# Kernel tuning notes

Hardware: AMD Instinct MI355X
Metric: run time of the kernel (lower is better)

## Reference

```python
import jax, jax.numpy as jnp
import numpy as np

EPS = 1e-5          # InstanceNorm eps (torch default)
KERNEL = 25         # moving_avg_kernel_size
TAU = 1.0           # gumbel softmax temperature
REGIME_NUM = 8


def _inorm(x):
    # InstanceNorm1d without affine on (N, C, L): normalize over last dim (biased var)
    m = x.mean(-1, keepdims=True)
    v = ((x - m) ** 2).mean(-1, keepdims=True)
    return (x - m) * jax.lax.rsqrt(v + EPS)


def _lbr(x, W, b):
    # Linear -> InstanceNorm (over last dim) -> exact GELU
    return jax.nn.gelu(_inorm(x @ W + b), approximate=False)


def _moving_avg(x, k):
    # x: (B, L, C); edge-replicate pad (k-1)//2 on both sides, sliding mean via cumsum
    p = (k - 1) // 2
    xp = jnp.concatenate([jnp.repeat(x[:, :1], p, axis=1), x,
                          jnp.repeat(x[:, -1:], p, axis=1)], axis=1)
    cs = jnp.concatenate([jnp.zeros_like(xp[:, :1]), jnp.cumsum(xp, axis=1)], axis=1)
    return (cs[:, k:] - cs[:, :-k]) / k  # (B, L, C)


def _encode(x, Ws, bs, Wt, bt):
    # inputs - inputs[:, 0:1]; series decomposition; seasonal+trend branches
    x = x - x[:, :1]
    mm = _moving_avg(x, KERNEL)
    return _lbr(x - mm, Ws, bs) + _lbr(mm, Wt, bt)  # (B, L, H)


def reference(inputs_longterm, inputs_shortterm,
              Ws, bs, Wt, bt,
              Wh1, bh1, Wl1, bl1, Wh2, bh2, Wl2, bl2, Wh3, bh3, Wl3, bl3,
              Wr, br, proto):
    e_lt = _encode(inputs_longterm, Ws, bs, Wt, bt)   # (B, L_lt, H)
    e_st = _encode(inputs_shortterm, Ws, bs, Wt, bt)  # (B, L_st, H)

    # RegimeEncoder: alternate hidden-dim and lookback-dim LinearBatchRelu layers
    o = _lbr(e_lt, Wh1, bh1)
    o = jnp.swapaxes(_lbr(jnp.swapaxes(o, 1, 2), Wl1, bl1), 1, 2)
    o = _lbr(o, Wh2, bh2)
    o = jnp.swapaxes(_lbr(jnp.swapaxes(o, 1, 2), Wl2, bl2), 1, 2)
    o = _lbr(o, Wh3, bh3)
    o = jnp.swapaxes(_lbr(jnp.swapaxes(o, 1, 2), Wl3, bl3), 1, 2)  # (B, L_lt//8, H)
    logits = o.reshape(o.shape[0], -1) @ Wr + br  # (B, R)

    # gumbel_softmax(hard=True) with straight-through estimator
    g = jax.random.gumbel(jax.random.key(42), logits.shape, logits.dtype)
    y_soft = jax.nn.softmax((logits + g) / TAU, axis=-1)
    y_hard = jax.nn.one_hot(jnp.argmax(y_soft, axis=-1), REGIME_NUM, dtype=logits.dtype)
    w = y_hard - jax.lax.stop_gradient(y_soft) + y_soft  # (B, R)

    # weighted sum over regime prototypes, then combine with encoded shortterm
    sel = jnp.einsum('br,rnhmo->bnhmo', w, proto)          # (B, L_st, H, M, 3)
    out = jnp.einsum('bnh,bnhmo->bmo', e_st, sel)          # (B, M, 3)
    B = out.shape[0]
    return jax.nn.softmax(out.reshape(B, -1), axis=-1).reshape(out.shape)


def setup_inputs() -> dict:
    key = jax.random.key(0)
    ks = jax.random.split(key, 24)
    B, L_lt, L_st, C, H, R, M = 32, 512, 128, 9, 128, 8, 64
    s = 0.02
    d = {
        'inputs_longterm':  jax.random.normal(ks[0], (B, L_lt, C), jnp.float32),
        'inputs_shortterm': jax.random.normal(ks[1], (B, L_st, C), jnp.float32),
        'Ws': jax.random.normal(ks[2], (C, H), jnp.float32) * s,
        'bs': jnp.zeros((H,), jnp.float32),
        'Wt': jax.random.normal(ks[3], (C, H), jnp.float32) * s,
        'bt': jnp.zeros((H,), jnp.float32),
        'Wh1': jax.random.normal(ks[4], (H, H), jnp.float32) * s,
        'bh1': jnp.zeros((H,), jnp.float32),
        'Wl1': jax.random.normal(ks[5], (L_lt, L_lt // 2), jnp.float32) * s,
        'bl1': jnp.zeros((L_lt // 2,), jnp.float32),
        'Wh2': jax.random.normal(ks[6], (H, H), jnp.float32) * s,
        'bh2': jnp.zeros((H,), jnp.float32),
        'Wl2': jax.random.normal(ks[7], (L_lt // 2, L_lt // 4), jnp.float32) * s,
        'bl2': jnp.zeros((L_lt // 4,), jnp.float32),
        'Wh3': jax.random.normal(ks[8], (H, H), jnp.float32) * s,
        'bh3': jnp.zeros((H,), jnp.float32),
        'Wl3': jax.random.normal(ks[9], (L_lt // 4, L_lt // 8), jnp.float32) * s,
        'bl3': jnp.zeros((L_lt // 8,), jnp.float32),
        'Wr': jax.random.normal(ks[10], (H * L_lt // 8, R), jnp.float32) * s,
        'br': jnp.zeros((R,), jnp.float32),
        'proto': jax.random.normal(ks[11], (R, L_st, H, M, 3), jnp.float32),
    }
    return d
```

## Files before the change

### kernel.cpp

```cpp
#include <hip/hip_runtime.h>
#include <math.h>

#define EPS 1e-5f

__device__ __forceinline__ float gelu_exact(float x) {
    return 0.5f * x * (1.0f + erff(x * 0.7071067811865476f));
}

__device__ float block_sum(float v, float* red) {
    int lane = threadIdx.x & 63, wid = threadIdx.x >> 6;
#pragma unroll
    for (int off = 32; off > 0; off >>= 1) v += __shfl_down(v, off, 64);
    if (lane == 0) red[wid] = v;
    __syncthreads();
    int nw = ((int)blockDim.x + 63) >> 6;
    float s = red[0];
    for (int w = 1; w < nw; w++) s += red[w];
    __syncthreads();
    return s;
}

__device__ float block_max(float v, float* red) {
    int lane = threadIdx.x & 63, wid = threadIdx.x >> 6;
#pragma unroll
    for (int off = 32; off > 0; off >>= 1) v = fmaxf(v, __shfl_down(v, off, 64));
    if (lane == 0) red[wid] = v;
    __syncthreads();
    int nw = ((int)blockDim.x + 63) >> 6;
    float s = red[0];
    for (int w = 1; w < nw; w++) s = fmaxf(s, red[w]);
    __syncthreads();
    return s;
}

__device__ void threefry2x32(unsigned k0, unsigned k1, unsigned x0, unsigned x1,
                             unsigned& o0, unsigned& o1) {
    unsigned ks[3] = {k0, k1, k0 ^ k1 ^ 0x1BD11BDAu};
    const unsigned rot[2][4] = {{13u, 15u, 26u, 6u}, {17u, 29u, 16u, 24u}};
    x0 += ks[0]; x1 += ks[1];
#pragma unroll
    for (int i = 0; i < 5; i++) {
#pragma unroll
        for (int j = 0; j < 4; j++) {
            unsigned r = rot[i & 1][j];
            x0 += x1;
            x1 = (x1 << r) | (x1 >> (32 - r));
            x1 ^= x0;
        }
        x0 += ks[(i + 1) % 3];
        x1 += ks[(i + 2) % 3] + (unsigned)(i + 1);
    }
    o0 = x0; o1 = x1;
}

__device__ float gumbel_at(int j) {
    unsigned o0, o1;
    threefry2x32(0u, 42u, 0u, (unsigned)j, o0, o1);
    unsigned bits = o0 ^ o1;
    float f = __uint_as_float((bits >> 9) | 0x3F800000u) - 1.0f;
    float u = fmaxf(f + 1.17549435e-38f, 1.17549435e-38f);
    return -logf(-logf(u));
}

__device__ void bsum2_128(float& a, float& b, float (*red)[2]) {
    int lane = threadIdx.x & 63, wid = threadIdx.x >> 6;
#pragma unroll
    for (int off = 32; off > 0; off >>= 1) {
        a += __shfl_xor(a, off, 64);
        b += __shfl_xor(b, off, 64);
    }
    if (lane == 0) { red[wid][0] = a; red[wid][1] = b; }
    __syncthreads();
    a = red[0][0] + red[1][0];
    b = red[0][1] + red[1][1];
}

__global__ void encode_kernel(const float* __restrict__ x_lt, const float* __restrict__ x_st,
                              const float* __restrict__ Ws, const float* __restrict__ bs,
                              const float* __restrict__ Wt, const float* __restrict__ bt,
                              float* __restrict__ e_lt, float* __restrict__ e_st) {
    const int H = 128;
    int b = blockIdx.y, t = threadIdx.x;
    const float* x;
    float* e;
    int L, l;
    if (blockIdx.x < 512) { x = x_lt; e = e_lt; L = 512; l = blockIdx.x; }
    else { x = x_st; e = e_st; L = 128; l = blockIdx.x - 512; }
    __shared__ float part[117];
    __shared__ float seas[9], mmv[9];
    __shared__ float redA[2][2], redB[2][2];
    const float* xb = x + (size_t)b * L * 9;
    if (t < 117) {
        int c = t / 13, g = t % 13;
        int lj0 = l + 2 * g - 12;
        lj0 = lj0 < 0 ? 0 : (lj0 >= L ? L - 1 : lj0);
        float s = xb[(size_t)lj0 * 9 + c];
        if (g < 12) {
            int lj1 = l + 2 * g - 11;
            lj1 = lj1 < 0 ? 0 : (lj1 >= L ? L - 1 : lj1);
            s += xb[(size_t)lj1 * 9 + c];
        }
        part[t] = s;
    }
    __syncthreads();
    if (t < 9) {
        float s = 0.f;
        for (int g = 0; g < 13; g++) s += part[t * 13 + g];
        float x0 = xb[t];
        float mm = (s - 25.f * x0) * (1.0f / 25.0f);
        float xd = xb[(size_t)l * 9 + t] - x0;
        mmv[t] = mm;
        seas[t] = xd - mm;
    }
    __syncthreads();
    float ys = bs[t], yt = bt[t];
#pragma unroll
    for (int c = 0; c < 9; c++) {
        ys += seas[c] * Ws[c * H + t];
        yt += mmv[c] * Wt[c * H + t];
    }
    float sa = ys, sb = yt;
    bsum2_128(sa, sb, redA);
    float ms = sa * (1.0f / 128.0f), mt = sb * (1.0f / 128.0f);
    float ds = ys - ms, dt = yt - mt;
    float qa = ds * ds, qb = dt * dt;
    bsum2_128(qa, qb, redB);
    float gy = gelu_exact(ds * rsqrtf(qa * (1.0f / 128.0f) + EPS));
    float gt = gelu_exact(dt * rsqrtf(qb * (1.0f / 128.0f) + EPS));
    e[((size_t)b * L + l) * H + t] = gy + gt;
}

template <int K, int N, int WR, bool TRANS>
__global__ __launch_bounds__(256) void lbr_wave(
    const float* __restrict__ A, int S, int ABOFF,
    const float* __restrict__ W, const float* __restrict__ bias,
    float* __restrict__ out, int OROWS, int OBOFF) {
    constexpr int CG = N / 4;
    constexpr int SG = 64 / CG;
    constexpr int RW = SG * WR;
    constexpr int MT = 4 * RW;
    constexpr int LOG2MT = (MT == 8) ? 3 : ((MT == 16) ? 4 : 5);
    constexpr int STAGE = 4 * RW * K;
    constexpr int TILE = TRANS ? MT * (N + 4) : 0;
    constexpr int LSZ = STAGE > TILE ? STAGE : TILE;
    __shared__ float lds[LSZ];
    const int t = threadIdx.x;
    const int w = t >> 6, ln = t & 63;
    const int sg = ln / CG;
    const int n0 = (ln % CG) * 4;
    const int b = blockIdx.y;
    const int r0b = blockIdx.x * MT;
    const int r0w = r0b + w * RW;
    float* As = lds + w * RW * K;
    const float* Ab = A + (size_t)b * ABOFF;
    for (int idx = ln; idx < RW * (K / 4); idx += 64) {
        int rr = idx / (K / 4), kk = idx % (K / 4);
        float4 v = *(const float4*)(Ab + (size_t)(r0w + rr) * S + kk * 4);
        *(float4*)(As + rr * K + kk * 4) = v;
    }
    float4 acc[WR];
    {
        float4 bv = *(const float4*)(bias + n0);
#pragma unroll
        for (int j = 0; j < WR; j++) acc[j] = bv;
    }
    const float* ap = As + (sg * WR) * K;
    const float* wp = W + n0;
#pragma unroll 8
    for (int k = 0; k < K; k++) {
        float4 wv = *(const float4*)wp;
        wp += N;
#pragma unroll
        for (int j = 0; j < WR; j++) {
            float a = ap[j * K + k];
            acc[j].x += a * wv.x;
            acc[j].y += a * wv.y;
            acc[j].z += a * wv.z;
            acc[j].w += a * wv.w;
        }
    }
    float4 res[WR];
#pragma unroll
    for (int j = 0; j < WR; j++) {
        float s = acc[j].x + acc[j].y + acc[j].z + acc[j].w;
#pragma unroll
        for (int off = CG / 2; off > 0; off >>= 1) s += __shfl_xor(s, off, 64);
        float m = s * (1.0f / (float)N);
        float dx = acc[j].x - m, dy = acc[j].y - m, dz = acc[j].z - m, dw = acc[j].w - m;
        float q = dx * dx + dy * dy + dz * dz + dw * dw;
#pragma unroll
        for (int off = CG / 2; off > 0; off >>= 1) q += __shfl_xor(q, off, 64);
        float inv = rsqrtf(q * (1.0f / (float)N) + EPS);
        res[j].x = gelu_exact(dx * inv);
        res[j].y = gelu_exact(dy * inv);
        res[j].z = gelu_exact(dz * inv);
        res[j].w = gelu_exact(dw * inv);
    }
    if constexpr (TRANS) {
        __syncthreads();
#pragma unroll
        for (int j = 0; j < WR; j++) {
            int rl = w * RW + sg * WR + j;
            *(float4*)(lds + rl * (N + 4) + n0) = res[j];
        }
        __syncthreads();
        float* ob = out + (size_t)b * OBOFF + r0b;
        for (int e = t; e < MT * N; e += 256) {
            int r = e & (MT - 1), n = e >> LOG2MT;
            ob[(size_t)n * OROWS + r] = lds[r * (N + 4) + n];
        }
    } else {
        float* ob = out + (size_t)b * OBOFF;
#pragma unroll
        for (int j = 0; j < WR; j++) {
            int row = r0w + sg * WR + j;
            *(float4*)(ob + (size_t)row * N + n0) = res[j];
        }
    }
}

__global__ void logits_part(const float* __restrict__ O6, const float* __restrict__ Wr,
                            float* __restrict__ part_lg) {
    int s = blockIdx.x, b = blockIdx.y, t = threadIdx.x;
    const float* ob = O6 + (size_t)b * 8192;
    float acc[8] = {0, 0, 0, 0, 0, 0, 0, 0};
#pragma unroll
    for (int q = 0; q < 4; q++) {
        int i = s * 1024 + q * 256 + t;
        int l4 = i >> 7, h = i & 127;
        float v = ob[h * 64 + l4];
        const float* wr = Wr + (size_t)i * 8;
#pragma unroll
        for (int j = 0; j < 8; j++) acc[j] += v * wr[j];
    }
#pragma unroll
    for (int j = 0; j < 8; j++)
#pragma unroll
        for (int off = 32; off > 0; off >>= 1) acc[j] += __shfl_xor(acc[j], off, 64);
    __shared__ float red[4][8];
    int lane = t & 63, wid = t >> 6;
    if (lane == 0)
        for (int j = 0; j < 8; j++) red[wid][j] = acc[j];
    __syncthreads();
    if (t < 8)
        part_lg[((size_t)s * 32 + b) * 8 + t] = red[0][t] + red[1][t] + red[2][t] + red[3][t];
}

__global__ void select_kernel(const float* __restrict__ part_lg, const float* __restrict__ br,
                              float* __restrict__ sel_w, int* __restrict__ sel_r,
                              int* __restrict__ cnt, int* __restrict__ list) {
    int t = threadIdx.x;
    __shared__ int s_r[32];
    if (t < 32) {
        float z[8];
        for (int j = 0; j < 8; j++) {
            float lg = br[j];
            for (int s = 0; s < 8; s++) lg += part_lg[((size_t)s * 32 + t) * 8 + j];
            z[j] = lg + gumbel_at(t * 8 + j);
        }
        int am = 0;
        float zm = z[0];
        for (int j = 1; j < 8; j++)
            if (z[j] > zm) { zm = z[j]; am = j; }
        float ssum = 0.f;
        for (int j = 0; j < 8; j++) ssum += expf(z[j] - zm);
        float s = 1.0f / ssum;
        sel_w[t] = (1.0f - s) + s;
        sel_r[t] = am;
        s_r[t] = am;
    }
    __syncthreads();
    if (t == 0) {
        int c[8] = {0, 0, 0, 0, 0, 0, 0, 0};
        for (int b = 0; b < 32; b++) {
            int r = s_r[b];
            list[r * 32 + c[r]] = b;
            c[r]++;
        }
        for (int r = 0; r < 8; r++) cnt[r] = c[r];
    }
}

__global__ void einsum_nsplit(const float* __restrict__ e_st, const float* __restrict__ proto,
                              const int* __restrict__ cnt, const int* __restrict__ list,
                              float* __restrict__ part) {
    int n = blockIdx.x, r = blockIdx.y, t = threadIdx.x;
    int gs = cnt[r];
    if (gs == 0) return;
    __shared__ float es[8][128];
    const float* pb = proto + ((size_t)r * 128 + n) * 128 * 192;
    for (int s0 = 0; s0 < gs; s0 += 8) {
        int np = gs - s0 < 8 ? gs - s0 : 8;
        __syncthreads();
        for (int i = t; i < 1024; i += 192) {
            int sb = i >> 7, h = i & 127;
            if (sb < np) {
                int b = list[r * 32 + s0 + sb];
                es[sb][h] = e_st[((size_t)b * 128 + n) * 128 + h];
            } else {
                es[sb][h] = 0.f;
            }
        }
        __syncthreads();
        float a0 = 0.f, a1 = 0.f, a2 = 0.f, a3 = 0.f;
        float a4 = 0.f, a5 = 0.f, a6 = 0.f, a7 = 0.f;
#pragma unroll 8
        for (int h = 0; h < 128; h++) {
            float p = pb[h * 192 + t];
            a0 += es[0][h] * p; a1 += es[1][h] * p;
            a2 += es[2][h] * p; a3 += es[3][h] * p;
            a4 += es[4][h] * p; a5 += es[5][h] * p;
            a6 += es[6][h] * p; a7 += es[7][h] * p;
        }
        float av[8] = {a0, a1, a2, a3, a4, a5, a6, a7};
#pragma unroll
        for (int sb = 0; sb < 8; sb++) {
            if (sb < np) {
                int b = list[r * 32 + s0 + sb];
                part[((size_t)b * 128 + n) * 192 + t] = av[sb];
            }
        }
    }
}

__global__ void finalize_kernel(const float* __restrict__ part, const float* __restrict__ sel_w,
                                float* __restrict__ out) {
    int b = blockIdx.x, t = threadIdx.x;
    __shared__ float red[4];
    float v = 0.f;
#pragma unroll 8
    for (int c = 0; c < 128; c++) v += part[((size_t)b * 128 + c) * 192 + t];
    v *= sel_w[b];
    float mx = block_max(v, red);
    float e = expf(v - mx);
    float s = block_sum(e, red);
    out[(size_t)b * 192 + t] = e / s;
}

extern "C" void kernel_launch(void* const* d_in, const int* in_sizes, int n_in,
                              void* d_out, int out_size, void* d_ws, size_t ws_size,
                              hipStream_t stream) {
    const float* in_lt = (const float*)d_in[0];
    const float* in_st = (const float*)d_in[1];
    const float* Ws  = (const float*)d_in[2];  const float* bs  = (const float*)d_in[3];
    const float* Wt  = (const float*)d_in[4];  const float* bt  = (const float*)d_in[5];
    const float* Wh1 = (const float*)d_in[6];  const float* bh1 = (const float*)d_in[7];
    const float* Wl1 = (const float*)d_in[8];  const float* bl1 = (const float*)d_in[9];
    const float* Wh2 = (const float*)d_in[10]; const float* bh2 = (const float*)d_in[11];
    const float* Wl2 = (const float*)d_in[12]; const float* bl2 = (const float*)d_in[13];
    const float* Wh3 = (const float*)d_in[14]; const float* bh3 = (const float*)d_in[15];
    const float* Wl3 = (const float*)d_in[16]; const float* bl3 = (const float*)d_in[17];
    const float* Wr  = (const float*)d_in[18]; const float* br  = (const float*)d_in[19];
    const float* proto = (const float*)d_in[20];
    float* out = (float*)d_out;

    float* ws = (float*)d_ws;
    size_t off = 0;
    float* e_lt = ws + off; off += (size_t)32 * 512 * 128;
    float* e_st = ws + off; off += (size_t)32 * 128 * 128;
    float* O1T = ws + off; off += (size_t)128 * 16384;
    float* O2T = ws + off; off += (size_t)256 * 4096;
    float* O3T = ws + off; off += (size_t)128 * 8192;
    float* O4T = ws + off; off += (size_t)128 * 4096;
    float* O5T = ws + off; off += (size_t)128 * 4096;
    float* O6 = ws + off; off += (size_t)32 * 128 * 64;
    float* part = ws + off; off += (size_t)32 * 128 * 192;
    float* part_lg = ws + off; off += 8 * 32 * 8;
    float* sel_w = ws + off; off += 32;
    int* sel_r = (int*)(ws + off); off += 32;
    int* cnt = (int*)(ws + off); off += 8;
    int* list = (int*)(ws + off); off += 256;

    encode_kernel<<<dim3(640, 32), 128, 0, stream>>>(in_lt, in_st, Ws, bs, Wt, bt, e_lt, e_st);
    lbr_wave<128, 128, 2, true><<<dim3(1024, 1), 256, 0, stream>>>(
        e_lt, 128, 0, Wh1, bh1, O1T, 16384, 0);
    lbr_wave<512, 256, 2, true><<<dim3(16, 32), 256, 0, stream>>>(
        O1T, 16384, 512, Wl1, bl1, O2T, 4096, 128);
    lbr_wave<128, 128, 2, true><<<dim3(16, 32), 256, 0, stream>>>(
        O2T, 4096, 128, Wh2, bh2, O3T, 8192, 256);
    lbr_wave<256, 128, 1, true><<<dim3(16, 32), 256, 0, stream>>>(
        O3T, 8192, 256, Wl2, bl2, O4T, 4096, 128);
    lbr_wave<128, 128, 1, true><<<dim3(16, 32), 256, 0, stream>>>(
        O4T, 4096, 128, Wh3, bh3, O5T, 4096, 128);
    lbr_wave<128, 64, 1, false><<<dim3(8, 32), 256, 0, stream>>>(
        O5T, 4096, 128, Wl3, bl3, O6, 0, 8192);
    logits_part<<<dim3(8, 32), 256, 0, stream>>>(O6, Wr, part_lg);
    select_kernel<<<1, 64, 0, stream>>>(part_lg, br, sel_w, sel_r, cnt, list);
    einsum_nsplit<<<dim3(128, 8), 192, 0, stream>>>(e_st, proto, cnt, list, part);
    finalize_kernel<<<32, 192, 0, stream>>>(part, sel_w, out);
}
```

Baseline: 363.0 us.

## Fuse logits and regime selection; build per-regime lists inside einsum; retile LBR layers

Merges the split-K logits kernel and the single-block selection kernel into one kernel per batch row that computes the full logits reduction and gumbel argmax. Each einsum block now builds its own list of batches for its regime from sel_r in shared memory, so the serial list-building kernel goes away. Four lbr_wave launches double their per-block row count and halve the grid. Together these remove a launch and a serial step, at the cost of less parallelism in the logits reduction and fewer blocks for the middle layers.

```diff
diff --git a/kernel.cpp b/kernel.cpp
--- a/kernel.cpp
+++ b/kernel.cpp
@@ -219,14 +219,15 @@
     }
 }
 
-__global__ void logits_part(const float* __restrict__ O6, const float* __restrict__ Wr,
-                            float* __restrict__ part_lg) {
-    int s = blockIdx.x, b = blockIdx.y, t = threadIdx.x;
+__global__ void logits_select(const float* __restrict__ O6, const float* __restrict__ Wr,
+                              const float* __restrict__ br,
+                              float* __restrict__ sel_w, int* __restrict__ sel_r) {
+    int b = blockIdx.x, t = threadIdx.x;
     const float* ob = O6 + (size_t)b * 8192;
     float acc[8] = {0, 0, 0, 0, 0, 0, 0, 0};
-#pragma unroll
-    for (int q = 0; q < 4; q++) {
-        int i = s * 1024 + q * 256 + t;
+#pragma unroll 4
+    for (int q = 0; q < 32; q++) {
+        int i = q * 256 + t;
         int l4 = i >> 7, h = i & 127;
         float v = ob[h * 64 + l4];
         const float* wr = Wr + (size_t)i * 8;
@@ -242,21 +243,11 @@
     if (lane == 0)
         for (int j = 0; j < 8; j++) red[wid][j] = acc[j];
     __syncthreads();
-    if (t < 8)
-        part_lg[((size_t)s * 32 + b) * 8 + t] = red[0][t] + red[1][t] + red[2][t] + red[3][t];
-}
-
-__global__ void select_kernel(const float* __restrict__ part_lg, const float* __restrict__ br,
-                              float* __restrict__ sel_w, int* __restrict__ sel_r,
-                              int* __restrict__ cnt, int* __restrict__ list) {
-    int t = threadIdx.x;
-    __shared__ int s_r[32];
-    if (t < 32) {
+    if (t == 0) {
         float z[8];
         for (int j = 0; j < 8; j++) {
-            float lg = br[j];
-            for (int s = 0; s < 8; s++) lg += part_lg[((size_t)s * 32 + t) * 8 + j];
-            z[j] = lg + gumbel_at(t * 8 + j);
+            float lg = br[j] + red[0][j] + red[1][j] + red[2][j] + red[3][j];
+            z[j] = lg + gumbel_at(b * 8 + j);
         }
         int am = 0;
         float zm = z[0];
@@ -265,27 +256,24 @@
         float ssum = 0.f;
         for (int j = 0; j < 8; j++) ssum += expf(z[j] - zm);
         float s = 1.0f / ssum;
-        sel_w[t] = (1.0f - s) + s;
-        sel_r[t] = am;
-        s_r[t] = am;
-    }
-    __syncthreads();
+        sel_w[b] = (1.0f - s) + s;
+        sel_r[b] = am;
+    }
+}
+
+__global__ void einsum_nsplit(const float* __restrict__ e_st, const float* __restrict__ proto,
+                              const int* __restrict__ sel_r, float* __restrict__ part) {
+    int n = blockIdx.x, r = blockIdx.y, t = threadIdx.x;
+    __shared__ int loc[32];
+    __shared__ int s_gs;
     if (t == 0) {
-        int c[8] = {0, 0, 0, 0, 0, 0, 0, 0};
-        for (int b = 0; b < 32; b++) {
-            int r = s_r[b];
-            list[r * 32 + c[r]] = b;
-            c[r]++;
-        }
-        for (int r = 0; r < 8; r++) cnt[r] = c[r];
-    }
-}
-
-__global__ void einsum_nsplit(const float* __restrict__ e_st, const float* __restrict__ proto,
-                              const int* __restrict__ cnt, const int* __restrict__ list,
-                              float* __restrict__ part) {
-    int n = blockIdx.x, r = blockIdx.y, t = threadIdx.x;
-    int gs = cnt[r];
+        int g = 0;
+        for (int bb = 0; bb < 32; bb++)
+            if (sel_r[bb] == r) loc[g++] = bb;
+        s_gs = g;
+    }
+    __syncthreads();
+    int gs = s_gs;
     if (gs == 0) return;
     __shared__ float es[8][128];
     const float* pb = proto + ((size_t)r * 128 + n) * 128 * 192;
@@ -295,7 +283,7 @@
         for (int i = t; i < 1024; i += 192) {
             int sb = i >> 7, h = i & 127;
             if (sb < np) {
-                int b = list[r * 32 + s0 + sb];
+                int b = loc[s0 + sb];
                 es[sb][h] = e_st[((size_t)b * 128 + n) * 128 + h];
             } else {
                 es[sb][h] = 0.f;
@@ -316,7 +304,7 @@
 #pragma unroll
         for (int sb = 0; sb < 8; sb++) {
             if (sb < np) {
-                int b = list[r * 32 + s0 + sb];
+                int b = loc[s0 + sb];
                 part[((size_t)b * 128 + n) * 192 + t] = av[sb];
             }
         }
@@ -365,27 +353,23 @@
     float* O5T = ws + off; off += (size_t)128 * 4096;
     float* O6 = ws + off; off += (size_t)32 * 128 * 64;
     float* part = ws + off; off += (size_t)32 * 128 * 192;
-    float* part_lg = ws + off; off += 8 * 32 * 8;
     float* sel_w = ws + off; off += 32;
     int* sel_r = (int*)(ws + off); off += 32;
-    int* cnt = (int*)(ws + off); off += 8;
-    int* list = (int*)(ws + off); off += 256;
 
     encode_kernel<<<dim3(640, 32), 128, 0, stream>>>(in_lt, in_st, Ws, bs, Wt, bt, e_lt, e_st);
     lbr_wave<128, 128, 2, true><<<dim3(1024, 1), 256, 0, stream>>>(
         e_lt, 128, 0, Wh1, bh1, O1T, 16384, 0);
-    lbr_wave<512, 256, 2, true><<<dim3(16, 32), 256, 0, stream>>>(
+    lbr_wave<512, 256, 4, true><<<dim3(8, 32), 256, 0, stream>>>(
         O1T, 16384, 512, Wl1, bl1, O2T, 4096, 128);
-    lbr_wave<128, 128, 2, true><<<dim3(16, 32), 256, 0, stream>>>(
+    lbr_wave<128, 128, 4, true><<<dim3(8, 32), 256, 0, stream>>>(
         O2T, 4096, 128, Wh2, bh2, O3T, 8192, 256);
-    lbr_wave<256, 128, 1, true><<<dim3(16, 32), 256, 0, stream>>>(
+    lbr_wave<256, 128, 2, true><<<dim3(8, 32), 256, 0, stream>>>(
         O3T, 8192, 256, Wl2, bl2, O4T, 4096, 128);
-    lbr_wave<128, 128, 1, true><<<dim3(16, 32), 256, 0, stream>>>(
+    lbr_wave<128, 128, 2, true><<<dim3(8, 32), 256, 0, stream>>>(
         O4T, 4096, 128, Wh3, bh3, O5T, 4096, 128);
     lbr_wave<128, 64, 1, false><<<dim3(8, 32), 256, 0, stream>>>(
         O5T, 4096, 128, Wl3, bl3, O6, 0, 8192);
-    logits_part<<<dim3(8, 32), 256, 0, stream>>>(O6, Wr, part_lg);
-    select_kernel<<<1, 64, 0, stream>>>(part_lg, br, sel_w, sel_r, cnt, list);
-    einsum_nsplit<<<dim3(128, 8), 192, 0, stream>>>(e_st, proto, cnt, list, part);
+    logits_select<<<32, 256, 0, stream>>>(O6, Wr, br, sel_w, sel_r);
+    einsum_nsplit<<<dim3(128, 8), 192, 0, stream>>>(e_st, proto, sel_r, part);
     finalize_kernel<<<32, 192, 0, stream>>>(part, sel_w, out);
 }
```

New measurement: 378.7 us. +4.3%, slower.
